# Kernel tuning notes

Measured on AMD Instinct MI355X. Metric: run time of the kernel, lower is better.

The kernel has to match this reference:

```python
import jax, jax.numpy as jnp
import numpy as np

B, L, D, H, M = 2, 4096, 1024, 16, 256
DH = D // H
EPS = 1e-6
LN_EPS = 1e-5


def setup_inputs() -> dict:
    key = jax.random.key(0)
    ks = jax.random.split(key, 6)
    inp = {
        "x": jax.random.normal(ks[0], (B, L, D), jnp.float32),
        "Wq": jax.random.normal(ks[1], (D, D), jnp.float32) * (D ** -0.5),
        "Wk": jax.random.normal(ks[2], (D, D), jnp.float32) * (D ** -0.5),
        "Wv": jax.random.normal(ks[3], (D, D), jnp.float32) * (D ** -0.5),
        "Wo": jax.random.normal(ks[4], (D, D), jnp.float32) * (D ** -0.5),
        "proj": jax.random.normal(ks[5], (H, M, DH), jnp.float32),
        "ln_g": jnp.ones((D,), jnp.float32),
        "ln_b": jnp.zeros((D,), jnp.float32),
        "scale_factor": 2,
    }
    return inp


def _heads(t, W):
    b, l, _ = t.shape
    return (t @ W).reshape(b, l, H, DH).transpose(0, 2, 1, 3)  # bhld


def _favor_features(u, proj):
    # u: [B,H,L,DH] already scaled by d_head**-0.25; proj: [H,M,DH]
    dash = jnp.einsum("bhld,hmd->bhlm", u, proj)
    diag = 0.5 * jnp.sum(u * u, axis=-1, keepdims=True)  # [B,H,L,1]
    stab = jnp.max(dash, axis=-1, keepdims=True)
    return jnp.exp(dash - diag - stab) * (M ** -0.5)  # [B,H,L,M]


def reference(x, Wq, Wk, Wv, Wo, proj, ln_g, ln_b, scale_factor):
    b, l, d = x.shape
    # nearest-neighbor upsample along sequence (F.interpolate default mode)
    up = jnp.repeat(x, scale_factor, axis=1)  # [B, L*s, D]

    scale = DH ** -0.25
    q = _heads(up, Wq) * scale   # [B,H,Lq,DH]
    k = _heads(x, Wk) * scale    # [B,H,L,DH]
    v = _heads(x, Wv)            # [B,H,L,DH]

    qf = _favor_features(q, proj)  # [B,H,Lq,M]
    kf = _favor_features(k, proj)  # [B,H,L,M]

    kv = jnp.einsum("bhlm,bhld->bhmd", kf, v)          # [B,H,M,DH]
    k_sum = jnp.sum(kf, axis=2)                          # [B,H,M]
    z = 1.0 / (jnp.einsum("bhlm,bhm->bhl", qf, k_sum) + EPS)
    attn = jnp.einsum("bhlm,bhmd->bhld", qf, kv) * z[..., None]

    lq = attn.shape[2]
    y = attn.transpose(0, 2, 1, 3).reshape(b, lq, d) @ Wo
    y = jax.nn.gelu(y, approximate=False)

    mu = jnp.mean(y, axis=-1, keepdims=True)
    var = jnp.mean((y - mu) ** 2, axis=-1, keepdims=True)
    return (y - mu) * jax.lax.rsqrt(var + LN_EPS) * ln_g + ln_b
```

## Files before the change

kernel.cpp:

```cpp
#include <hip/hip_runtime.h>

static constexpr int kB  = 2;
static constexpr int kL  = 4096;
static constexpr int kD  = 1024;
static constexpr int kH  = 16;
static constexpr int kDH = 64;
static constexpr int kM  = 256;
static constexpr int kN  = kB * kL;
static constexpr float kScale    = 0.35355339059327373f;
static constexpr float kInvSqrtM = 0.0625f;
static constexpr float kEps   = 1e-6f;
static constexpr float kLnEps = 1e-5f;

typedef __attribute__((ext_vector_type(8))) short short8;
typedef __attribute__((ext_vector_type(4))) float f32x4;

__device__ __forceinline__ float bf2f(unsigned short h) {
  union { unsigned int u; float f; } c;
  c.u = ((unsigned int)h) << 16;
  return c.f;
}
__device__ __forceinline__ unsigned short f2bf(float f) {
  union { float f; unsigned int u; } c;
  c.f = f;
  unsigned int u = c.u;
  u += 0x7fffu + ((u >> 16) & 1u);
  return (unsigned short)(u >> 16);
}

__global__ __launch_bounds__(256) void cast_bf16_kernel(
    const float* __restrict__ in, unsigned short* __restrict__ out)
{
  const int i = blockIdx.x * 256 + threadIdx.x;
  float4 v = ((const float4*)in)[i];
  ushort4 o;
  o.x = f2bf(v.x); o.y = f2bf(v.y); o.z = f2bf(v.z); o.w = f2bf(v.w);
  ((ushort4*)out)[i] = o;
}

__global__ __launch_bounds__(256) void transpose_cast_kernel(
    const float* __restrict__ W, unsigned short* __restrict__ WT)
{
  __shared__ float tile[32][33];
  const int n0 = blockIdx.x * 32, k0 = blockIdx.y * 32;
  const int t = threadIdx.x, kk = t >> 5, nn = t & 31;
#pragma unroll
  for (int i = 0; i < 4; ++i)
    tile[kk + i * 8][nn] = W[(size_t)(k0 + kk + i * 8) * kD + n0 + nn];
  __syncthreads();
#pragma unroll
  for (int i = 0; i < 4; ++i)
    WT[(size_t)(n0 + kk + i * 8) * kD + k0 + nn] = f2bf(tile[nn][kk + i * 8]);
}

template <int OUT_MODE>
__global__ __launch_bounds__(256) void gemm_mfma(
    const unsigned short* __restrict__ A, const unsigned short* __restrict__ BT,
    void* __restrict__ Cout, float alpha)
{
  __shared__ unsigned short sm[2 * 128 * 40];
  unsigned short* As = sm;
  unsigned short* Bs = sm + 128 * 40;
  const int tid = threadIdx.x, lane = tid & 63, w = tid >> 6;
  const int q = lane >> 4, c = lane & 15;
  const int wr = (w >> 1) * 64, wc = (w & 1) * 64;
  const int row0 = blockIdx.y * 128, col0 = blockIdx.x * 128;
  const int trow = tid >> 2, tc8 = (tid & 3) * 8;

  f32x4 acc[4][4];
#pragma unroll
  for (int i = 0; i < 4; ++i)
#pragma unroll
    for (int j = 0; j < 4; ++j) acc[i][j] = (f32x4)0.f;

  for (int k0 = 0; k0 < kD; k0 += 32) {
    __syncthreads();
#pragma unroll
    for (int i = 0; i < 2; ++i) {
      *(uint4*)&As[(trow + 64 * i) * 40 + tc8] =
          *(const uint4*)&A[(size_t)(row0 + trow + 64 * i) * kD + k0 + tc8];
      *(uint4*)&Bs[(trow + 64 * i) * 40 + tc8] =
          *(const uint4*)&BT[(size_t)(col0 + trow + 64 * i) * kD + k0 + tc8];
    }
    __syncthreads();
    short8 av[4], bv[4];
#pragma unroll
    for (int i = 0; i < 4; ++i)
      av[i] = *(const short8*)&As[(wr + i * 16 + c) * 40 + q * 8];
#pragma unroll
    for (int j = 0; j < 4; ++j)
      bv[j] = *(const short8*)&Bs[(wc + j * 16 + c) * 40 + q * 8];
#pragma unroll
    for (int i = 0; i < 4; ++i)
#pragma unroll
      for (int j = 0; j < 4; ++j)
        acc[i][j] = __builtin_amdgcn_mfma_f32_16x16x32_bf16(
            av[i], bv[j], acc[i][j], 0, 0, 0);
  }

  if (OUT_MODE != 2) {
#pragma unroll
    for (int i = 0; i < 4; ++i)
#pragma unroll
      for (int j = 0; j < 4; ++j)
#pragma unroll
        for (int r = 0; r < 4; ++r) {
          const int row = row0 + wr + i * 16 + q * 4 + r;
          const int col = col0 + wc + j * 16 + c;
          const float v = alpha * acc[i][j][r];
          if (OUT_MODE == 1)
            ((unsigned short*)Cout)[(size_t)row * kD + col] = f2bf(v);
          else
            ((float*)Cout)[(size_t)row * kD + col] = v;
        }
  } else {
    unsigned short* T = sm;
    const int bq = row0 >> 12, l0 = row0 & 4095;
    __syncthreads();
#pragma unroll
    for (int hh = 0; hh < 2; ++hh) {
      if ((w & 1) == hh) {
#pragma unroll
        for (int i = 0; i < 4; ++i)
#pragma unroll
          for (int j = 0; j < 4; ++j) {
            ushort4 o;
            o.x = f2bf(acc[i][j][0]); o.y = f2bf(acc[i][j][1]);
            o.z = f2bf(acc[i][j][2]); o.w = f2bf(acc[i][j][3]);
            *(ushort4*)&T[(j * 16 + c) * 136 + wr + i * 16 + q * 4] = o;
          }
      }
      __syncthreads();
      {
        const int dl = tid >> 2, seg = tid & 3;
        const size_t dst =
            ((size_t)(bq * 1024 + col0 + hh * 64 + dl)) * (size_t)kL +
            l0 + seg * 32;
        uint4* gp = (uint4*)((unsigned short*)Cout + dst);
        const unsigned short* sp = &T[dl * 136 + seg * 32];
#pragma unroll
        for (int u = 0; u < 4; ++u) gp[u] = *(const uint4*)&sp[u * 8];
      }
      __syncthreads();
    }
  }
}

template <int TRANS>
__global__ __launch_bounds__(256) void favor_mfma(
    const unsigned short* __restrict__ U, const unsigned short* __restrict__ projb,
    unsigned short* __restrict__ F)
{
  __shared__ unsigned short Us[128 * 72];
  __shared__ unsigned short Ps[256 * 72];
  __shared__ float diagp[256];
  __shared__ float diag[128];
  const int bh = blockIdx.x, b = bh >> 4, h = bh & 15;
  const int l0 = blockIdx.y * 128;
  const int tid = threadIdx.x, lane = tid & 63, w = tid >> 6;
  const int q = lane >> 4, c = lane & 15;
  const int wr = w * 32;

#pragma unroll
  for (int it = 0; it < 4; ++it) {
    int idx = it * 256 + tid;
    int row = idx >> 3, col8 = idx & 7;
    *(uint4*)&Us[row * 72 + col8 * 8] =
        *(const uint4*)&U[((size_t)(b * kL + l0 + row)) * kD + h * kDH + col8 * 8];
  }
#pragma unroll
  for (int it = 0; it < 8; ++it) {
    int idx = it * 256 + tid;
    int row = idx >> 3, col8 = idx & 7;
    *(uint4*)&Ps[row * 72 + col8 * 8] =
        *(const uint4*)&projb[((size_t)h * kM + row) * kDH + col8 * 8];
  }
  __syncthreads();

  {
    int row = tid & 127, half = tid >> 7;
    const unsigned short* ur = &Us[row * 72 + half * 32];
    float s = 0.f;
#pragma unroll
    for (int d8 = 0; d8 < 4; ++d8) {
      uint4 raw = *(const uint4*)&ur[d8 * 8];
      const unsigned short* us = (const unsigned short*)&raw;
#pragma unroll
      for (int j = 0; j < 8; ++j) { float v = bf2f(us[j]); s = fmaf(v, v, s); }
    }
    diagp[half * 128 + row] = s;
  }

  f32x4 acc[2][16];
#pragma unroll
  for (int i = 0; i < 2; ++i)
#pragma unroll
    for (int j = 0; j < 16; ++j) acc[i][j] = (f32x4)0.f;

#pragma unroll
  for (int ks = 0; ks < 2; ++ks) {
    short8 av[2];
#pragma unroll
    for (int i = 0; i < 2; ++i)
      av[i] = *(const short8*)&Us[(wr + i * 16 + c) * 72 + ks * 32 + q * 8];
#pragma unroll
    for (int j = 0; j < 16; ++j) {
      short8 bv = *(const short8*)&Ps[(j * 16 + c) * 72 + ks * 32 + q * 8];
#pragma unroll
      for (int i = 0; i < 2; ++i)
        acc[i][j] = __builtin_amdgcn_mfma_f32_16x16x32_bf16(
            av[i], bv, acc[i][j], 0, 0, 0);
    }
  }

  __syncthreads();
  if (tid < 128) diag[tid] = 0.5f * (diagp[tid] + diagp[128 + tid]);
  __syncthreads();

#pragma unroll
  for (int i = 0; i < 2; ++i)
#pragma unroll
    for (int r = 0; r < 4; ++r) {
      const int lrow = wr + i * 16 + q * 4 + r;
      float mx = -3.4e38f;
#pragma unroll
      for (int j = 0; j < 16; ++j) mx = fmaxf(mx, acc[i][j][r]);
      mx = fmaxf(mx, __shfl_xor(mx, 1, 64));
      mx = fmaxf(mx, __shfl_xor(mx, 2, 64));
      mx = fmaxf(mx, __shfl_xor(mx, 4, 64));
      mx = fmaxf(mx, __shfl_xor(mx, 8, 64));
      const float base = diag[lrow] + mx;
      if (TRANS == 0) {
        const size_t gbase = ((size_t)bh * kL + (l0 + lrow)) * kM;
#pragma unroll
        for (int j = 0; j < 16; ++j)
          F[gbase + j * 16 + c] = f2bf(__expf(acc[i][j][r] - base) * kInvSqrtM);
      } else {
#pragma unroll
        for (int j = 0; j < 16; ++j)
          acc[i][j][r] = __expf(acc[i][j][r] - base) * kInvSqrtM;
      }
    }

  if (TRANS == 1) {
    unsigned short* T = Ps;
    __syncthreads();
#pragma unroll
    for (int mc = 0; mc < 2; ++mc) {
#pragma unroll
      for (int i = 0; i < 2; ++i)
#pragma unroll
        for (int jl = 0; jl < 8; ++jl) {
          const int jj = mc * 8 + jl;
          ushort4 o;
          o.x = f2bf(acc[i][jj][0]); o.y = f2bf(acc[i][jj][1]);
          o.z = f2bf(acc[i][jj][2]); o.w = f2bf(acc[i][jj][3]);
          *(ushort4*)&T[(jl * 16 + c) * 136 + wr + i * 16 + q * 4] = o;
        }
      __syncthreads();
      {
        const int ml = tid >> 1, seg = tid & 1;
        const size_t dst =
            ((size_t)(bh * kM + mc * 128 + ml)) * (size_t)kL + l0 + seg * 64;
        uint4* gp = (uint4*)(F + dst);
        const unsigned short* sp = &T[ml * 136 + seg * 64];
#pragma unroll
        for (int u = 0; u < 8; ++u) gp[u] = *(const uint4*)&sp[u * 8];
      }
      __syncthreads();
    }
  }
}

__global__ __launch_bounds__(256) void kv_mfma(
    const unsigned short* __restrict__ KFT, const unsigned short* __restrict__ VT,
    float* __restrict__ KVP, float* __restrict__ KSP)
{
  __shared__ unsigned short As[128 * 40];
  __shared__ unsigned short Bs[64 * 40];
  const int bh = blockIdx.x, mtile = blockIdx.y, split = blockIdx.z;
  const int tid = threadIdx.x, lane = tid & 63, w = tid >> 6;
  const int q = lane >> 4, c = lane & 15;
  const int l0 = split * 512;
  const unsigned short* Abase = KFT + ((size_t)(bh * kM + mtile * 128)) * kL + l0;
  const unsigned short* Bbase = VT + ((size_t)(bh * kDH)) * kL + l0;

  f32x4 acc[2][4];
#pragma unroll
  for (int i = 0; i < 2; ++i)
#pragma unroll
    for (int j = 0; j < 4; ++j) acc[i][j] = (f32x4)0.f;
  float ksr[2] = {0.f, 0.f};

  for (int k0 = 0; k0 < 512; k0 += 32) {
    __syncthreads();
#pragma unroll
    for (int it = 0; it < 2; ++it) {
      int idx = it * 256 + tid;
      int row = idx >> 2, c8 = (idx & 3) * 8;
      *(uint4*)&As[row * 40 + c8] = *(const uint4*)&Abase[(size_t)row * kL + k0 + c8];
    }
    {
      int row = tid >> 2, c8 = (tid & 3) * 8;
      *(uint4*)&Bs[row * 40 + c8] = *(const uint4*)&Bbase[(size_t)row * kL + k0 + c8];
    }
    __syncthreads();
    short8 av[2], bv[4];
#pragma unroll
    for (int i = 0; i < 2; ++i) {
      av[i] = *(const short8*)&As[(w * 32 + i * 16 + c) * 40 + q * 8];
#pragma unroll
      for (int e = 0; e < 8; ++e) ksr[i] += bf2f((unsigned short)av[i][e]);
    }
#pragma unroll
    for (int j = 0; j < 4; ++j)
      bv[j] = *(const short8*)&Bs[(j * 16 + c) * 40 + q * 8];
#pragma unroll
    for (int i = 0; i < 2; ++i)
#pragma unroll
      for (int j = 0; j < 4; ++j)
        acc[i][j] = __builtin_amdgcn_mfma_f32_16x16x32_bf16(
            av[i], bv[j], acc[i][j], 0, 0, 0);
  }

  const int blk = (bh * 2 + mtile) * 8 + split;
  float* op = KVP + (size_t)blk * (128 * 64);
#pragma unroll
  for (int i = 0; i < 2; ++i)
#pragma unroll
    for (int j = 0; j < 4; ++j)
#pragma unroll
      for (int r = 0; r < 4; ++r)
        op[(w * 32 + i * 16 + q * 4 + r) * 64 + j * 16 + c] = acc[i][j][r];

#pragma unroll
  for (int i = 0; i < 2; ++i) {
    float s = ksr[i];
    s += __shfl_xor(s, 16, 64);
    s += __shfl_xor(s, 32, 64);
    if (q == 0) KSP[blk * 128 + w * 32 + i * 16 + c] = s;
  }
}

__global__ __launch_bounds__(256) void kv_reduce_kernel(
    const float* __restrict__ KVP, const float* __restrict__ KSP,
    unsigned short* __restrict__ KVT)
{
  const int blk = blockIdx.x;
  const int bh = blk / 80, n = blk - bh * 80;
  const int t = threadIdx.x;
  const int mt = t >> 7, ml = t & 127;
  float s = 0.f;
  if (n < 64) {
#pragma unroll
    for (int sp = 0; sp < 8; ++sp)
      s += KVP[((size_t)((bh * 2 + mt) * 8 + sp)) * (128 * 64) + ml * 64 + n];
  } else if (n == 64) {
#pragma unroll
    for (int sp = 0; sp < 8; ++sp)
      s += KSP[((bh * 2 + mt) * 8 + sp) * 128 + ml];
  }
  KVT[(size_t)bh * (80 * kM) + n * kM + t] = f2bf(s);
}

__global__ __launch_bounds__(256) void attn_mfma(
    const unsigned short* __restrict__ QF, const unsigned short* __restrict__ KVT,
    unsigned short* __restrict__ ATTN)
{
  __shared__ unsigned short kvs[80 * 264];
  __shared__ unsigned short qs[128 * 40];
  const int bh = blockIdx.x, b = bh >> 4, h = bh & 15;
  const int l0 = blockIdx.y * 128;
  const int tid = threadIdx.x, lane = tid & 63, w = tid >> 6;
  const int q = lane >> 4, c = lane & 15;
  const int trow = tid >> 2, tc8 = (tid & 3) * 8;

#pragma unroll
  for (int it = 0; it < 20; ++it) {
    int idx4 = it * 256 + tid;
    int row = idx4 >> 6, col4 = idx4 & 63;
    *(ushort4*)&kvs[row * 264 + col4 * 4] =
        *(const ushort4*)&KVT[(size_t)bh * (80 * kM) + row * kM + col4 * 4];
  }

  f32x4 acc[2][5];
#pragma unroll
  for (int i = 0; i < 2; ++i)
#pragma unroll
    for (int j = 0; j < 5; ++j) acc[i][j] = (f32x4)0.f;

  for (int kk = 0; kk < 8; ++kk) {
    __syncthreads();
#pragma unroll
    for (int i = 0; i < 2; ++i)
      *(uint4*)&qs[(trow + 64 * i) * 40 + tc8] =
          *(const uint4*)&QF[((size_t)bh * kL + (l0 + trow + 64 * i)) * kM +
                             kk * 32 + tc8];
    __syncthreads();
    short8 bv[5];
#pragma unroll
    for (int j = 0; j < 5; ++j)
      bv[j] = *(const short8*)&kvs[(j * 16 + c) * 264 + kk * 32 + q * 8];
#pragma unroll
    for (int i = 0; i < 2; ++i) {
      short8 av = *(const short8*)&qs[(w * 32 + i * 16 + c) * 40 + q * 8];
#pragma unroll
      for (int j = 0; j < 5; ++j)
        acc[i][j] = __builtin_amdgcn_mfma_f32_16x16x32_bf16(
            av, bv[j], acc[i][j], 0, 0, 0);
    }
  }

#pragma unroll
  for (int i = 0; i < 2; ++i)
#pragma unroll
    for (int r = 0; r < 4; ++r) {
      float den = __shfl(acc[i][4][r], (lane & 48));
      float z = 1.f / (den + kEps);
      const int row = l0 + w * 32 + i * 16 + q * 4 + r;
      const size_t base = ((size_t)(b * kL + row)) * kD + h * kDH;
#pragma unroll
      for (int j = 0; j < 4; ++j)
        ATTN[base + j * 16 + c] = f2bf(acc[i][j][r] * z);
    }
}

__global__ __launch_bounds__(256) void gelu_ln_kernel(
    const float* __restrict__ Y, const float* __restrict__ lng,
    const float* __restrict__ lnb, float* __restrict__ OUT)
{
  __shared__ float r1[4], r2[4];
  const int n = blockIdx.x;
  const int tid = threadIdx.x, lane = tid & 63, w = tid >> 6;

  float4 y4 = ((const float4*)(Y + (size_t)n * kD))[tid];
  float g0 = 0.5f * y4.x * (1.f + erff(y4.x * 0.70710678118654752f));
  float g1 = 0.5f * y4.y * (1.f + erff(y4.y * 0.70710678118654752f));
  float g2 = 0.5f * y4.z * (1.f + erff(y4.z * 0.70710678118654752f));
  float g3 = 0.5f * y4.w * (1.f + erff(y4.w * 0.70710678118654752f));

  float s  = (g0 + g1) + (g2 + g3);
  float ss = (g0 * g0 + g1 * g1) + (g2 * g2 + g3 * g3);
#pragma unroll
  for (int off = 32; off; off >>= 1) {
    s  += __shfl_xor(s, off, 64);
    ss += __shfl_xor(ss, off, 64);
  }
  if (lane == 0) { r1[w] = s; r2[w] = ss; }
  __syncthreads();
  s  = (r1[0] + r1[1]) + (r1[2] + r1[3]);
  ss = (r2[0] + r2[1]) + (r2[2] + r2[3]);
  float mu  = s * (1.f / (float)kD);
  float var = ss * (1.f / (float)kD) - mu * mu;
  float inv = rsqrtf(var + kLnEps);

  float4 gg = ((const float4*)lng)[tid];
  float4 bb = ((const float4*)lnb)[tid];
  float4 o;
  o.x = (g0 - mu) * inv * gg.x + bb.x;
  o.y = (g1 - mu) * inv * gg.y + bb.y;
  o.z = (g2 - mu) * inv * gg.z + bb.z;
  o.w = (g3 - mu) * inv * gg.w + bb.w;

  const int b = n >> 12, l = n & 4095;
  const int cc = tid * 4;
  size_t base = ((size_t)(b * 8192 + 2 * l)) * kD + cc;
  *(float4*)(OUT + base)      = o;
  *(float4*)(OUT + base + kD) = o;
}

extern "C" void kernel_launch(void* const* d_in, const int* in_sizes, int n_in,
                              void* d_out, int out_size, void* d_ws, size_t ws_size,
                              hipStream_t stream)
{
  (void)in_sizes; (void)n_in; (void)out_size; (void)ws_size;
  const float* x    = (const float*)d_in[0];
  const float* Wq   = (const float*)d_in[1];
  const float* Wk   = (const float*)d_in[2];
  const float* Wv   = (const float*)d_in[3];
  const float* Wo   = (const float*)d_in[4];
  const float* proj = (const float*)d_in[5];
  const float* lng  = (const float*)d_in[6];
  const float* lnb  = (const float*)d_in[7];
  float* out = (float*)d_out;

  char* ws = (char*)d_ws;
  const size_t MB = 1024 * 1024;
  unsigned short* xb  = (unsigned short*)(ws);
  unsigned short* WqT = (unsigned short*)(ws + 16 * MB);
  unsigned short* WkT = (unsigned short*)(ws + 18 * MB);
  unsigned short* WvT = (unsigned short*)(ws + 20 * MB);
  unsigned short* WoT = (unsigned short*)(ws + 22 * MB);
  unsigned short* Qb  = (unsigned short*)(ws + 24 * MB);
  unsigned short* Kb  = (unsigned short*)(ws + 40 * MB);
  unsigned short* VT  = (unsigned short*)(ws + 56 * MB);
  unsigned short* QF  = (unsigned short*)(ws + 72 * MB);
  unsigned short* KFT = (unsigned short*)(ws + 136 * MB);
  float* KSP          = (float*)(ws + 200 * MB);
  unsigned short* KVT = (unsigned short*)(ws + 201 * MB);
  unsigned short* projb = (unsigned short*)(ws + 203 * MB);
  float* KVP          = (float*)(ws + 24 * MB);
  unsigned short* ATTN = Kb;
  float* Y            = (float*)(ws + 72 * MB);

  cast_bf16_kernel<<<(kN * kD) / 1024, 256, 0, stream>>>(x, xb);
  cast_bf16_kernel<<<(kH * kM * kDH) / 1024, 256, 0, stream>>>(proj, projb);
  transpose_cast_kernel<<<dim3(32, 32), 256, 0, stream>>>(Wq, WqT);
  transpose_cast_kernel<<<dim3(32, 32), 256, 0, stream>>>(Wk, WkT);
  transpose_cast_kernel<<<dim3(32, 32), 256, 0, stream>>>(Wv, WvT);
  transpose_cast_kernel<<<dim3(32, 32), 256, 0, stream>>>(Wo, WoT);

  dim3 gg(8, 64);
  gemm_mfma<1><<<gg, 256, 0, stream>>>(xb, WkT, Kb, kScale);
  gemm_mfma<2><<<gg, 256, 0, stream>>>(xb, WvT, VT, 1.0f);
  gemm_mfma<1><<<gg, 256, 0, stream>>>(xb, WqT, Qb, kScale);

  favor_mfma<0><<<dim3(32, 32), 256, 0, stream>>>(Qb, projb, QF);
  favor_mfma<1><<<dim3(32, 32), 256, 0, stream>>>(Kb, projb, KFT);

  kv_mfma<<<dim3(32, 2, 8), 256, 0, stream>>>(KFT, VT, KVP, KSP);
  kv_reduce_kernel<<<32 * 80, 256, 0, stream>>>(KVP, KSP, KVT);

  attn_mfma<<<dim3(32, 32), 256, 0, stream>>>(QF, KVT, ATTN);

  gemm_mfma<0><<<gg, 256, 0, stream>>>(ATTN, WoT, Y, 1.0f);

  gelu_ln_kernel<<<kN, 256, 0, stream>>>(Y, lng, lnb, out);
}
```

Measured before the change: 396.8 us.

## Use direct global-to-LDS loads in GEMM and read proj from global in favor

The GEMM tile loads now use global_load_lds, which writes global data straight into unpadded LDS and skips the register round trip. The trailing barrier moves to the end of each k-step, and the transpose buffer gets its own allocation. The favor kernel stops staging the projection matrix in LDS and loads its MFMA operands directly from global memory, relying on cache. It also shrinks the transpose staging buffer and writes out in four chunks, cutting LDS use so more blocks fit per CU. The risks are bank conflicts from the unpadded 32-wide LDS rows and extra global and L2 traffic for proj.

```diff
diff --git a/kernel.cpp b/kernel.cpp
--- a/kernel.cpp
+++ b/kernel.cpp
@@ -28,6 +28,13 @@
   return (unsigned short)(u >> 16);
 }
 
+__device__ __forceinline__ void gload_lds16(const unsigned short* g,
+                                            unsigned short* l) {
+  __builtin_amdgcn_global_load_lds(
+      (const __attribute__((address_space(1))) unsigned int*)g,
+      (__attribute__((address_space(3))) unsigned int*)l, 16, 0, 0);
+}
+
 __global__ __launch_bounds__(256) void cast_bf16_kernel(
     const float* __restrict__ in, unsigned short* __restrict__ out)
 {
@@ -58,14 +65,14 @@
     const unsigned short* __restrict__ A, const unsigned short* __restrict__ BT,
     void* __restrict__ Cout, float alpha)
 {
-  __shared__ unsigned short sm[2 * 128 * 40];
-  unsigned short* As = sm;
-  unsigned short* Bs = sm + 128 * 40;
+  __shared__ unsigned short As[128 * 32];
+  __shared__ unsigned short Bs[128 * 32];
+  __shared__ unsigned short Tbuf[OUT_MODE == 2 ? 64 * 136 : 1];
   const int tid = threadIdx.x, lane = tid & 63, w = tid >> 6;
   const int q = lane >> 4, c = lane & 15;
   const int wr = (w >> 1) * 64, wc = (w & 1) * 64;
   const int row0 = blockIdx.y * 128, col0 = blockIdx.x * 128;
-  const int trow = tid >> 2, tc8 = (tid & 3) * 8;
+  const int lrow = lane >> 2, lcol = (lane & 3) * 8;
 
   f32x4 acc[4][4];
 #pragma unroll
@@ -74,28 +81,27 @@
     for (int j = 0; j < 4; ++j) acc[i][j] = (f32x4)0.f;
 
   for (int k0 = 0; k0 < kD; k0 += 32) {
-    __syncthreads();
 #pragma unroll
     for (int i = 0; i < 2; ++i) {
-      *(uint4*)&As[(trow + 64 * i) * 40 + tc8] =
-          *(const uint4*)&A[(size_t)(row0 + trow + 64 * i) * kD + k0 + tc8];
-      *(uint4*)&Bs[(trow + 64 * i) * 40 + tc8] =
-          *(const uint4*)&BT[(size_t)(col0 + trow + 64 * i) * kD + k0 + tc8];
+      const int r0 = w * 32 + i * 16;
+      gload_lds16(&A[(size_t)(row0 + r0 + lrow) * kD + k0 + lcol], &As[r0 * 32]);
+      gload_lds16(&BT[(size_t)(col0 + r0 + lrow) * kD + k0 + lcol], &Bs[r0 * 32]);
     }
     __syncthreads();
     short8 av[4], bv[4];
 #pragma unroll
     for (int i = 0; i < 4; ++i)
-      av[i] = *(const short8*)&As[(wr + i * 16 + c) * 40 + q * 8];
+      av[i] = *(const short8*)&As[(wr + i * 16 + c) * 32 + q * 8];
 #pragma unroll
     for (int j = 0; j < 4; ++j)
-      bv[j] = *(const short8*)&Bs[(wc + j * 16 + c) * 40 + q * 8];
+      bv[j] = *(const short8*)&Bs[(wc + j * 16 + c) * 32 + q * 8];
 #pragma unroll
     for (int i = 0; i < 4; ++i)
 #pragma unroll
       for (int j = 0; j < 4; ++j)
         acc[i][j] = __builtin_amdgcn_mfma_f32_16x16x32_bf16(
             av[i], bv[j], acc[i][j], 0, 0, 0);
+    __syncthreads();
   }
 
   if (OUT_MODE != 2) {
@@ -114,9 +120,7 @@
             ((float*)Cout)[(size_t)row * kD + col] = v;
         }
   } else {
-    unsigned short* T = sm;
     const int bq = row0 >> 12, l0 = row0 & 4095;
-    __syncthreads();
 #pragma unroll
     for (int hh = 0; hh < 2; ++hh) {
       if ((w & 1) == hh) {
@@ -127,7 +131,7 @@
             ushort4 o;
             o.x = f2bf(acc[i][j][0]); o.y = f2bf(acc[i][j][1]);
             o.z = f2bf(acc[i][j][2]); o.w = f2bf(acc[i][j][3]);
-            *(ushort4*)&T[(j * 16 + c) * 136 + wr + i * 16 + q * 4] = o;
+            *(ushort4*)&Tbuf[(j * 16 + c) * 136 + wr + i * 16 + q * 4] = o;
           }
       }
       __syncthreads();
@@ -137,7 +141,7 @@
             ((size_t)(bq * 1024 + col0 + hh * 64 + dl)) * (size_t)kL +
             l0 + seg * 32;
         uint4* gp = (uint4*)((unsigned short*)Cout + dst);
-        const unsigned short* sp = &T[dl * 136 + seg * 32];
+        const unsigned short* sp = &Tbuf[dl * 136 + seg * 32];
 #pragma unroll
         for (int u = 0; u < 4; ++u) gp[u] = *(const uint4*)&sp[u * 8];
       }
@@ -152,7 +156,7 @@
     unsigned short* __restrict__ F)
 {
   __shared__ unsigned short Us[128 * 72];
-  __shared__ unsigned short Ps[256 * 72];
+  __shared__ unsigned short Tbuf[TRANS ? 64 * 136 : 1];
   __shared__ float diagp[256];
   __shared__ float diag[128];
   const int bh = blockIdx.x, b = bh >> 4, h = bh & 15;
@@ -168,13 +172,6 @@
     *(uint4*)&Us[row * 72 + col8 * 8] =
         *(const uint4*)&U[((size_t)(b * kL + l0 + row)) * kD + h * kDH + col8 * 8];
   }
-#pragma unroll
-  for (int it = 0; it < 8; ++it) {
-    int idx = it * 256 + tid;
-    int row = idx >> 3, col8 = idx & 7;
-    *(uint4*)&Ps[row * 72 + col8 * 8] =
-        *(const uint4*)&projb[((size_t)h * kM + row) * kDH + col8 * 8];
-  }
   __syncthreads();
 
   {
@@ -204,12 +201,18 @@
     for (int i = 0; i < 2; ++i)
       av[i] = *(const short8*)&Us[(wr + i * 16 + c) * 72 + ks * 32 + q * 8];
 #pragma unroll
-    for (int j = 0; j < 16; ++j) {
-      short8 bv = *(const short8*)&Ps[(j * 16 + c) * 72 + ks * 32 + q * 8];
-#pragma unroll
-      for (int i = 0; i < 2; ++i)
-        acc[i][j] = __builtin_amdgcn_mfma_f32_16x16x32_bf16(
-            av[i], bv, acc[i][j], 0, 0, 0);
+    for (int jb = 0; jb < 2; ++jb) {
+      short8 bv[8];
+#pragma unroll
+      for (int jl = 0; jl < 8; ++jl)
+        bv[jl] = *(const short8*)&projb[
+            ((size_t)(h * kM + (jb * 8 + jl) * 16 + c)) * kDH + ks * 32 + q * 8];
+#pragma unroll
+      for (int jl = 0; jl < 8; ++jl)
+#pragma unroll
+        for (int i = 0; i < 2; ++i)
+          acc[i][jb * 8 + jl] = __builtin_amdgcn_mfma_f32_16x16x32_bf16(
+              av[i], bv[jl], acc[i][jb * 8 + jl], 0, 0, 0);
     }
   }
 
@@ -243,31 +246,28 @@
     }
 
   if (TRANS == 1) {
-    unsigned short* T = Ps;
-    __syncthreads();
-#pragma unroll
-    for (int mc = 0; mc < 2; ++mc) {
-#pragma unroll
-      for (int i = 0; i < 2; ++i)
-#pragma unroll
-        for (int jl = 0; jl < 8; ++jl) {
-          const int jj = mc * 8 + jl;
+#pragma unroll
+    for (int mc = 0; mc < 4; ++mc) {
+      __syncthreads();
+#pragma unroll
+      for (int jl = 0; jl < 4; ++jl) {
+        const int jj = mc * 4 + jl;
+#pragma unroll
+        for (int i = 0; i < 2; ++i) {
           ushort4 o;
           o.x = f2bf(acc[i][jj][0]); o.y = f2bf(acc[i][jj][1]);
           o.z = f2bf(acc[i][jj][2]); o.w = f2bf(acc[i][jj][3]);
-          *(ushort4*)&T[(jl * 16 + c) * 136 + wr + i * 16 + q * 4] = o;
+          *(ushort4*)&Tbuf[(jl * 16 + c) * 136 + wr + i * 16 + q * 4] = o;
         }
-      __syncthreads();
-      {
-        const int ml = tid >> 1, seg = tid & 1;
-        const size_t dst =
-            ((size_t)(bh * kM + mc * 128 + ml)) * (size_t)kL + l0 + seg * 64;
-        uint4* gp = (uint4*)(F + dst);
-        const unsigned short* sp = &T[ml * 136 + seg * 64];
-#pragma unroll
-        for (int u = 0; u < 8; ++u) gp[u] = *(const uint4*)&sp[u * 8];
       }
       __syncthreads();
+#pragma unroll
+      for (int it = 0; it < 4; ++it) {
+        int idx = it * 256 + tid;
+        int row = idx >> 4, col8 = idx & 15;
+        *(uint4*)&F[((size_t)(bh * kM + mc * 64 + row)) * (size_t)kL +
+                    l0 + col8 * 8] = *(const uint4*)&Tbuf[row * 136 + col8 * 8];
+      }
     }
   }
 }
```

Measured after the change: 390.2 us. About the same (-1.7%).
